# Kernel optimization log

Hardware: AMD Instinct MI355X
Metric: run time of the kernel (lower is better)

## Reference

```python
import jax, jax.numpy as jnp
import numpy as np

N_NODES = 100000
N_EDGES = 1600000
IN_DIM = 256
HID_DIM = 64
NUM_CLASSES = 32
NEG_SLOPE = 0.01  # F.leaky_relu default


def setup_inputs() -> dict:
    key = jax.random.key(0)
    k1, k2, k3, k4, k5, k6 = jax.random.split(key, 6)
    return {
        "local_features": jax.random.normal(k1, (N_NODES, IN_DIM), dtype=jnp.float32),
        "edge_index": jax.random.randint(k2, (2, N_EDGES), 0, N_NODES, dtype=jnp.int64),
        "weight1": jax.random.uniform(k3, (IN_DIM, HID_DIM), dtype=jnp.float32),
        "weight2": jax.random.uniform(k4, (HID_DIM, NUM_CLASSES), dtype=jnp.float32),
        "att_weight1": jax.random.uniform(k5, (2 * HID_DIM, 1), dtype=jnp.float32),
        "att_weight2": jax.random.uniform(k6, (2 * NUM_CLASSES, 1), dtype=jnp.float32),
    }


def _gat_attention_aggregate(H, a, src, dst, n_nodes):
    # H: [N, D], a: [2D, 1]. Edge score = leaky_relu([H_src||H_dst] @ a)
    # computed without materializing [E, 2D]: split a into src/dst halves.
    d = H.shape[1]
    s_score = (H @ a[:d]).squeeze(-1)   # [N]
    d_score = (H @ a[d:]).squeeze(-1)   # [N]
    e = jax.nn.leaky_relu(s_score[src] + d_score[dst], NEG_SLOPE)  # [E]
    # segment softmax over each row (grouped by src), as torch.sparse.softmax(dim=1)
    m = jax.ops.segment_max(e, src, num_segments=n_nodes)          # [N]
    ex = jnp.exp(e - m[src])                                       # [E]
    denom = jax.ops.segment_sum(ex, src, num_segments=n_nodes)     # [N]
    att = ex / denom[src]                                          # [E]
    # sparse mm: out[i] = sum_{(i,j) in E} att_ij * H[j]
    return jax.ops.segment_sum(att[:, None] * H[dst], src, num_segments=n_nodes)


def reference(local_features, edge_index, weight1, weight2, att_weight1, att_weight2):
    src, dst = edge_index[0], edge_index[1]
    n = local_features.shape[0]
    Hw1 = local_features @ weight1                                  # [N, HID]
    hidden = jax.nn.elu(_gat_attention_aggregate(Hw1, att_weight1, src, dst, n))
    Hw2 = hidden @ weight2                                          # [N, C]
    out = _gat_attention_aggregate(Hw2, att_weight2, src, dst, n)
    return jax.nn.log_softmax(out, axis=1)
```

## Files before the change

### kernel.cpp

```cpp
#include <hip/hip_runtime.h>
#include <math.h>

#define IN_DIM 256
#define HID 64
#define NC 32
#define NEG 0.01f
#define INF_NEG -1e30f
#define SXR 68
#define MAXNBK 512
#define SLOT 8192
#define BCAP 12288

static inline int ceil_div(int a, int b){ return (a + b - 1) / b; }

static __device__ __forceinline__ float lrelu(float x){ return x > 0.f ? x : NEG * x; }


__global__ __launch_bounds__(256) void bin_kernel(const int* __restrict__ src,
      const int* __restrict__ dst, int* __restrict__ cursor,
      unsigned int* __restrict__ tmp, int E, int nbk){
  __shared__ int hist[MAXNBK];
  __shared__ int base[MAXNBK];
  int nb = gridDim.x;
  int per = (E + nb - 1) / nb;
  int beg = blockIdx.x * per;
  int end = min(E, beg + per);
  for (int i = threadIdx.x; i < nbk; i += 256) hist[i] = 0;
  __syncthreads();
  for (int e = beg + threadIdx.x; e < end; e += 256)
    atomicAdd(&hist[src[e] >> 8], 1);
  __syncthreads();
  for (int i = threadIdx.x; i < nbk; i += 256){
    int c = hist[i];
    base[i] = (c > 0) ? atomicAdd(&cursor[i], c) : 0;
    hist[i] = 0;
  }
  __syncthreads();
  for (int e = beg + threadIdx.x; e < end; e += 256){
    int s = src[e];
    int b = s >> 8;
    int r = atomicAdd(&hist[b], 1);
    int pos = base[b] + r;
    if (pos < SLOT)
      tmp[(size_t)b * SLOT + pos] = ((unsigned)(s & 255) << 17) | (unsigned)dst[e];
  }
}

__global__ __launch_bounds__(512) void bucket_base_kernel(const int* __restrict__ cursor,
      int* __restrict__ bbase, int nbk){
  __shared__ int sh[512];
  int tid = threadIdx.x;
  int v = (tid < nbk) ? min(cursor[tid], SLOT) : 0;
  sh[tid] = v; __syncthreads();
  int val = v;
  for (int off = 1; off < 512; off <<= 1){
    int add = (tid >= off) ? sh[tid - off] : 0;
    __syncthreads();
    val += add; sh[tid] = val;
    __syncthreads();
  }
  if (tid < nbk) bbase[tid] = val - v;
}

__global__ __launch_bounds__(256) void bucket_scatter_kernel(const unsigned int* __restrict__ tmp,
      const int* __restrict__ cursor, const int* __restrict__ bbase,
      int* __restrict__ row_ptr, int* __restrict__ csr, int n){
  __shared__ int cnt[256];
  __shared__ int cur[256];
  __shared__ int lbuf[BCAP];
  int tid = threadIdx.x;
  int b = blockIdx.x;
  int n0 = b << 8;
  int nn = min(256, n - n0);
  int len = min(cursor[b], SLOT);
  int segb = bbase[b];
  const unsigned int* T = tmp + (size_t)b * SLOT;
  cnt[tid] = 0;
  __syncthreads();
  for (int e = tid; e < len; e += 256) atomicAdd(&cnt[T[e] >> 17], 1);
  __syncthreads();
  int tv = cnt[tid];
  int val = tv;
  for (int off = 1; off < 256; off <<= 1){
    int add = (tid >= off) ? cnt[tid - off] : 0;
    __syncthreads();
    val += add; cnt[tid] = val;
    __syncthreads();
  }
  int excl = val - tv;
  cur[tid] = excl;
  if (tid < nn) row_ptr[n0 + tid] = segb + excl;
  if (n0 + nn == n && tid == 0) row_ptr[n] = segb + len;
  __syncthreads();
  if (len <= BCAP){
    for (int e = tid; e < len; e += 256){
      unsigned v = T[e];
      int pos = atomicAdd(&cur[v >> 17], 1);
      lbuf[pos] = (int)(v & 0x1FFFF);
    }
    __syncthreads();
    for (int e = tid; e < len; e += 256) csr[segb + e] = lbuf[e];
  } else {
    for (int e = tid; e < len; e += 256){
      unsigned v = T[e];
      int pos = atomicAdd(&cur[v >> 17], 1);
      csr[segb + pos] = (int)(v & 0x1FFFF);
    }
  }
}


__global__ void hist_kernel(const int* __restrict__ src, int* __restrict__ counts, int E){
  int i = blockIdx.x * blockDim.x + threadIdx.x;
  if (i < E) atomicAdd(&counts[src[i]], 1);
}
__global__ void scan_blocks_kernel(const int* __restrict__ counts, int* __restrict__ excl,
                                   int* __restrict__ bsums, int n){
  __shared__ int sh[256];
  int tid = threadIdx.x;
  int base = blockIdx.x * 1024 + tid * 4;
  int c[4]; int tsum = 0;
  #pragma unroll
  for (int j = 0; j < 4; j++){ int i = base + j; c[j] = (i < n) ? counts[i] : 0; tsum += c[j]; }
  sh[tid] = tsum; __syncthreads();
  int val = tsum;
  for (int off = 1; off < 256; off <<= 1){
    int add = (tid >= off) ? sh[tid - off] : 0;
    __syncthreads();
    val += add; sh[tid] = val;
    __syncthreads();
  }
  int p = val - tsum;
  #pragma unroll
  for (int j = 0; j < 4; j++){ int i = base + j; if (i < n) excl[i] = p; p += c[j]; }
  if (tid == 255) bsums[blockIdx.x] = val;
}
__global__ void scan_sums_kernel(int* __restrict__ bsums, int* __restrict__ row_ptr,
                                 int nb, int n, int E){
  __shared__ int sh[256];
  int tid = threadIdx.x;
  int v = (tid < nb) ? bsums[tid] : 0;
  sh[tid] = v; __syncthreads();
  int val = v;
  for (int off = 1; off < 256; off <<= 1){
    int add = (tid >= off) ? sh[tid - off] : 0;
    __syncthreads();
    val += add; sh[tid] = val;
    __syncthreads();
  }
  if (tid < nb) bsums[tid] = val - v;
  if (tid == 0) row_ptr[n] = E;
}
__global__ void add_offsets_kernel(int* __restrict__ excl, const int* __restrict__ bsums, int n){
  int i = blockIdx.x * 1024 + threadIdx.x;
  if (i < n) excl[i] += bsums[blockIdx.x];
}
__global__ void scatter_kernel(const int* __restrict__ src, const int* __restrict__ dst,
                               const int* __restrict__ row_ptr, int* __restrict__ fill,
                               int* __restrict__ csr, int E){
  int i = blockIdx.x * blockDim.x + threadIdx.x;
  if (i >= E) return;
  int s = src[i];
  int pos = row_ptr[s] + atomicAdd(&fill[s], 1);
  csr[pos] = dst[i];
}


__global__ __launch_bounds__(256) void gemm1_kernel(const float* __restrict__ X, const float* __restrict__ W,
      const float* __restrict__ a, float* __restrict__ H,
      float* __restrict__ svec, float* __restrict__ dvec, int n){
  __shared__ float xs[64 * SXR];
  __shared__ float ws[64 * 64];
  int tid = threadIdx.x;
  int r0 = blockIdx.x * 64;
  int tr = tid >> 4;
  int tc = tid & 15;
  int srow = tid >> 4, sc4 = tid & 15;

  float4 pfx[4], pfw[4];
  #pragma unroll
  for (int p = 0; p < 4; p++){
    int row = p * 16 + srow;
    int gr = r0 + row;
    pfx[p] = make_float4(0.f, 0.f, 0.f, 0.f);
    if (gr < n) pfx[p] = *(const float4*)(X + (size_t)gr * IN_DIM + sc4 * 4);
    int k = p * 16 + srow;
    pfw[p] = *(const float4*)(W + (size_t)k * 64 + sc4 * 4);
  }

  float acc[4][4];
  #pragma unroll
  for (int i = 0; i < 4; i++)
    #pragma unroll
    for (int j = 0; j < 4; j++) acc[i][j] = 0.f;

  for (int kb = 0; kb < 4; kb++){
    __syncthreads();
    #pragma unroll
    for (int p = 0; p < 4; p++){
      int row = p * 16 + srow;
      *(float4*)(xs + row * SXR + sc4 * 4) = pfx[p];
      int k = p * 16 + srow;
      *(float4*)(ws + k * 64 + sc4 * 4) = pfw[p];
    }
    if (kb < 3){
      #pragma unroll
      for (int p = 0; p < 4; p++){
        int row = p * 16 + srow;
        int gr = r0 + row;
        pfx[p] = make_float4(0.f, 0.f, 0.f, 0.f);
        if (gr < n) pfx[p] = *(const float4*)(X + (size_t)gr * IN_DIM + (kb + 1) * 64 + sc4 * 4);
        int k = p * 16 + srow;
        pfw[p] = *(const float4*)(W + (size_t)((kb + 1) * 64 + k) * 64 + sc4 * 4);
      }
    }
    __syncthreads();
    #pragma unroll 2
    for (int kq = 0; kq < 16; kq++){
      float xr[4][4];
      #pragma unroll
      for (int i = 0; i < 4; i++){
        float4 v = *(const float4*)(xs + (tr * 4 + i) * SXR + kq * 4);
        xr[i][0] = v.x; xr[i][1] = v.y; xr[i][2] = v.z; xr[i][3] = v.w;
      }
      #pragma unroll
      for (int dk = 0; dk < 4; dk++){
        float4 w4 = *(const float4*)(ws + (size_t)(kq * 4 + dk) * 64 + tc * 4);
        float wv[4] = {w4.x, w4.y, w4.z, w4.w};
        #pragma unroll
        for (int i = 0; i < 4; i++)
          #pragma unroll
          for (int j = 0; j < 4; j++) acc[i][j] = fmaf(xr[i][dk], wv[j], acc[i][j]);
      }
    }
  }

  float av[4], bv[4];
  #pragma unroll
  for (int j = 0; j < 4; j++){ av[j] = a[tc * 4 + j]; bv[j] = a[64 + tc * 4 + j]; }
  float sp[4], dp[4];
  #pragma unroll
  for (int i = 0; i < 4; i++){
    float s = 0.f, d = 0.f;
    #pragma unroll
    for (int j = 0; j < 4; j++){ s = fmaf(acc[i][j], av[j], s); d = fmaf(acc[i][j], bv[j], d); }
    sp[i] = s; dp[i] = d;
  }
  #pragma unroll
  for (int off = 1; off < 16; off <<= 1){
    #pragma unroll
    for (int i = 0; i < 4; i++){
      sp[i] += __shfl_xor(sp[i], off, 16);
      dp[i] += __shfl_xor(dp[i], off, 16);
    }
  }
  #pragma unroll
  for (int i = 0; i < 4; i++){
    int r = r0 + tr * 4 + i;
    if (r < n){
      *(float4*)(H + (size_t)r * 64 + tc * 4) = make_float4(acc[i][0], acc[i][1], acc[i][2], acc[i][3]);
      if (tc == 0){ svec[r] = sp[i]; dvec[r] = dp[i]; }
    }
  }
}


__global__ __launch_bounds__(256) void gemm2_kernel(const float* __restrict__ X, const float* __restrict__ W,
      const float* __restrict__ a, float* __restrict__ H,
      float* __restrict__ svec, float* __restrict__ dvec, int n){
  __shared__ float xs[64 * SXR];
  __shared__ float ws[64 * 32];
  int tid = threadIdx.x;
  int r0 = blockIdx.x * 64;
  int tr = tid >> 4;
  int tc = tid & 15;
  int srow = tid >> 4, sc4 = tid & 15;

  #pragma unroll
  for (int p = 0; p < 4; p++){
    int row = p * 16 + srow;
    int gr = r0 + row;
    float4 v = make_float4(0.f, 0.f, 0.f, 0.f);
    if (gr < n) v = *(const float4*)(X + (size_t)gr * HID + sc4 * 4);
    *(float4*)(xs + row * SXR + sc4 * 4) = v;
  }
  #pragma unroll
  for (int p = 0; p < 2; p++){
    int idx = p * 256 + tid;
    int k = idx >> 3, c4 = idx & 7;
    *(float4*)(ws + k * 32 + c4 * 4) = *(const float4*)(W + (size_t)k * 32 + c4 * 4);
  }
  __syncthreads();

  float acc[4][2];
  #pragma unroll
  for (int i = 0; i < 4; i++){ acc[i][0] = 0.f; acc[i][1] = 0.f; }

  #pragma unroll 2
  for (int kq = 0; kq < 16; kq++){
    float xr[4][4];
    #pragma unroll
    for (int i = 0; i < 4; i++){
      float4 v = *(const float4*)(xs + (tr * 4 + i) * SXR + kq * 4);
      xr[i][0] = v.x; xr[i][1] = v.y; xr[i][2] = v.z; xr[i][3] = v.w;
    }
    #pragma unroll
    for (int dk = 0; dk < 4; dk++){
      float2 w2 = *(const float2*)(ws + (size_t)(kq * 4 + dk) * 32 + tc * 2);
      #pragma unroll
      for (int i = 0; i < 4; i++){
        acc[i][0] = fmaf(xr[i][dk], w2.x, acc[i][0]);
        acc[i][1] = fmaf(xr[i][dk], w2.y, acc[i][1]);
      }
    }
  }

  float a0 = a[tc * 2], a1 = a[tc * 2 + 1];
  float b0 = a[32 + tc * 2], b1 = a[32 + tc * 2 + 1];
  float sp[4], dp[4];
  #pragma unroll
  for (int i = 0; i < 4; i++){
    sp[i] = fmaf(acc[i][0], a0, acc[i][1] * a1);
    dp[i] = fmaf(acc[i][0], b0, acc[i][1] * b1);
  }
  #pragma unroll
  for (int off = 1; off < 16; off <<= 1){
    #pragma unroll
    for (int i = 0; i < 4; i++){
      sp[i] += __shfl_xor(sp[i], off, 16);
      dp[i] += __shfl_xor(dp[i], off, 16);
    }
  }
  #pragma unroll
  for (int i = 0; i < 4; i++){
    int r = r0 + tr * 4 + i;
    if (r < n){
      *(float2*)(H + (size_t)r * NC + tc * 2) = make_float2(acc[i][0], acc[i][1]);
      if (tc == 0){ svec[r] = sp[i]; dvec[r] = dp[i]; }
    }
  }
}


__global__ __launch_bounds__(256) void agg1_kernel(const float* __restrict__ H, const float* __restrict__ sv,
      const float* __restrict__ dv, const int* __restrict__ row_ptr, const int* __restrict__ csr,
      float* __restrict__ out, int n){
  int t = blockIdx.x * 256 + threadIdx.x;
  int g = t >> 4, fl = t & 15;
  if (g >= n) return;
  int beg = row_ptr[g], end = row_ptr[g + 1];
  float si = sv[g];
  float m = INF_NEG, l = 0.f;
  float ox = 0.f, oy = 0.f, oz = 0.f, ow = 0.f;

  for (int cb = beg; cb < end; cb += 32){
    int ce = min(cb + 32, end);
    int e0 = cb + fl, e1 = cb + 16 + fl;
    int d0 = 0, d1 = 0;
    float ev0 = INF_NEG, ev1 = INF_NEG;
    if (e0 < ce){ d0 = csr[e0]; ev0 = lrelu(si + dv[d0]); }
    if (e1 < ce){ d1 = csr[e1]; ev1 = lrelu(si + dv[d1]); }
    float lm = fmaxf(ev0, ev1);
    #pragma unroll
    for (int off = 1; off < 16; off <<= 1) lm = fmaxf(lm, __shfl_xor(lm, off, 16));
    float nm = fmaxf(m, lm);
    float alpha = __expf(m - nm);
    m = nm;
    ev0 = __expf(ev0 - nm);
    ev1 = __expf(ev1 - nm);
    float ll = ev0 + ev1;
    #pragma unroll
    for (int off = 1; off < 16; off <<= 1) ll += __shfl_xor(ll, off, 16);
    l = l * alpha + ll;
    ox *= alpha; oy *= alpha; oz *= alpha; ow *= alpha;
    #pragma unroll
    for (int jj = 0; jj < 16; jj++){
      int e = cb + jj;
      if (e >= ce) break;
      float wgt = __shfl(ev0, jj, 16);
      int dd = __shfl(d0, jj, 16);
      float4 v = *(const float4*)(H + (size_t)dd * 64 + fl * 4);
      ox = fmaf(wgt, v.x, ox); oy = fmaf(wgt, v.y, oy);
      oz = fmaf(wgt, v.z, oz); ow = fmaf(wgt, v.w, ow);
    }
    #pragma unroll
    for (int jj = 0; jj < 16; jj++){
      int e = cb + 16 + jj;
      if (e >= ce) break;
      float wgt = __shfl(ev1, jj, 16);
      int dd = __shfl(d1, jj, 16);
      float4 v = *(const float4*)(H + (size_t)dd * 64 + fl * 4);
      ox = fmaf(wgt, v.x, ox); oy = fmaf(wgt, v.y, oy);
      oz = fmaf(wgt, v.z, oz); ow = fmaf(wgt, v.w, ow);
    }
  }
  float inv = (l > 0.f) ? 1.f / l : 0.f;
  ox *= inv; oy *= inv; oz *= inv; ow *= inv;
  ox = ox > 0.f ? ox : __expf(ox) - 1.f;
  oy = oy > 0.f ? oy : __expf(oy) - 1.f;
  oz = oz > 0.f ? oz : __expf(oz) - 1.f;
  ow = ow > 0.f ? ow : __expf(ow) - 1.f;
  *(float4*)(out + (size_t)g * 64 + fl * 4) = make_float4(ox, oy, oz, ow);
}


__global__ __launch_bounds__(256) void agg2_kernel(const float* __restrict__ H, const float* __restrict__ sv,
      const float* __restrict__ dv, const int* __restrict__ row_ptr, const int* __restrict__ csr,
      float* __restrict__ out, int n){
  int t = blockIdx.x * 256 + threadIdx.x;
  int g = t >> 3, fl = t & 7;
  if (g >= n) return;
  int beg = row_ptr[g], end = row_ptr[g + 1];
  float si = sv[g];
  float m = INF_NEG, l = 0.f;
  float ox = 0.f, oy = 0.f, oz = 0.f, ow = 0.f;

  for (int cb = beg; cb < end; cb += 32){
    int ce = min(cb + 32, end);
    float ev[4]; int dd4[4];
    float lm = INF_NEG;
    #pragma unroll
    for (int s = 0; s < 4; s++){
      int e = cb + s * 8 + fl;
      ev[s] = INF_NEG; dd4[s] = 0;
      if (e < ce){ dd4[s] = csr[e]; ev[s] = lrelu(si + dv[dd4[s]]); }
      lm = fmaxf(lm, ev[s]);
    }
    #pragma unroll
    for (int off = 1; off < 8; off <<= 1) lm = fmaxf(lm, __shfl_xor(lm, off, 8));
    float nm = fmaxf(m, lm);
    float alpha = __expf(m - nm);
    m = nm;
    float ll = 0.f;
    #pragma unroll
    for (int s = 0; s < 4; s++){ ev[s] = __expf(ev[s] - nm); ll += ev[s]; }
    #pragma unroll
    for (int off = 1; off < 8; off <<= 1) ll += __shfl_xor(ll, off, 8);
    l = l * alpha + ll;
    ox *= alpha; oy *= alpha; oz *= alpha; ow *= alpha;
    #pragma unroll
    for (int s = 0; s < 4; s++){
      #pragma unroll
      for (int jj = 0; jj < 8; jj++){
        int e = cb + s * 8 + jj;
        if (e >= ce) break;
        float wgt = __shfl(ev[s], jj, 8);
        int dd = __shfl(dd4[s], jj, 8);
        float4 v = *(const float4*)(H + (size_t)dd * 32 + fl * 4);
        ox = fmaf(wgt, v.x, ox); oy = fmaf(wgt, v.y, oy);
        oz = fmaf(wgt, v.z, oz); ow = fmaf(wgt, v.w, ow);
      }
    }
  }
  float inv = (l > 0.f) ? 1.f / l : 0.f;
  ox *= inv; oy *= inv; oz *= inv; ow *= inv;
  float tm = fmaxf(fmaxf(ox, oy), fmaxf(oz, ow));
  #pragma unroll
  for (int off = 1; off < 8; off <<= 1) tm = fmaxf(tm, __shfl_xor(tm, off, 8));
  float se = __expf(ox - tm) + __expf(oy - tm) + __expf(oz - tm) + __expf(ow - tm);
  #pragma unroll
  for (int off = 1; off < 8; off <<= 1) se += __shfl_xor(se, off, 8);
  float lg = tm + __logf(se);
  *(float4*)(out + (size_t)g * 32 + fl * 4) = make_float4(ox - lg, oy - lg, oz - lg, ow - lg);
}


extern "C" void kernel_launch(void* const* d_in, const int* in_sizes, int n_in,
                              void* d_out, int out_size, void* d_ws, size_t ws_size,
                              hipStream_t stream) {
  (void)n_in; (void)out_size; (void)ws_size;
  const float* X  = (const float*)d_in[0];
  const int*   EI = (const int*)d_in[1];
  const float* W1 = (const float*)d_in[2];
  const float* W2 = (const float*)d_in[3];
  const float* A1 = (const float*)d_in[4];
  const float* A2 = (const float*)d_in[5];
  float* out = (float*)d_out;

  int N = in_sizes[0] / IN_DIM;
  int E = in_sizes[1] / 2;
  const int* src = EI;
  const int* dst = EI + E;

  auto align_up = [](size_t x){ return (x + 511) & ~(size_t)511; };
  char* w = (char*)d_ws;
  int* counts  = (int*)w;   w += align_up((size_t)N * 4);
  int* cursor  = (int*)w;   w += align_up((size_t)MAXNBK * 4);
  int* bbase   = (int*)w;   w += align_up((size_t)MAXNBK * 4);
  int* row_ptr = (int*)w;   w += align_up((size_t)(N + 1) * 4);
  int* bsums   = (int*)w;   w += align_up(1024);
  int* csr     = (int*)w;   w += align_up((size_t)E * 4);
  float* H1    = (float*)w; w += align_up((size_t)N * 64 * 4);
  float* hid   = (float*)w; w += align_up((size_t)N * 64 * 4);
  float* s1    = (float*)w; w += align_up((size_t)N * 4);
  float* d1    = (float*)w; w += align_up((size_t)N * 4);
  float* s2    = (float*)w; w += align_up((size_t)N * 4);
  float* d2    = (float*)w; w += align_up((size_t)N * 4);
  float* H2    = H1;
  unsigned int* tmp = (unsigned int*)hid;

  int nbk = ceil_div(N, 256);

  if (N <= (1 << 17) && nbk <= MAXNBK && (size_t)nbk * SLOT <= (size_t)N * 64){
    hipMemsetAsync(cursor, 0, (size_t)nbk * 4, stream);
    bin_kernel<<<256, 256, 0, stream>>>(src, dst, cursor, tmp, E, nbk);
    bucket_base_kernel<<<1, 512, 0, stream>>>(cursor, bbase, nbk);
    bucket_scatter_kernel<<<nbk, 256, 0, stream>>>(tmp, cursor, bbase, row_ptr, csr, N);
  } else {
    int nb = ceil_div(N, 1024);
    hipMemsetAsync(counts, 0, (size_t)N * 4, stream);
    hist_kernel<<<ceil_div(E, 256), 256, 0, stream>>>(src, counts, E);
    scan_blocks_kernel<<<nb, 256, 0, stream>>>(counts, row_ptr, bsums, N);
    scan_sums_kernel<<<1, 256, 0, stream>>>(bsums, row_ptr, nb, N, E);
    add_offsets_kernel<<<nb, 1024, 0, stream>>>(row_ptr, bsums, N);
    hipMemsetAsync(counts, 0, (size_t)N * 4, stream);
    scatter_kernel<<<ceil_div(E, 256), 256, 0, stream>>>(src, dst, row_ptr, counts, csr, E);
  }

  gemm1_kernel<<<ceil_div(N, 64), 256, 0, stream>>>(X, W1, A1, H1, s1, d1, N);
  agg1_kernel<<<ceil_div(N * 16, 256), 256, 0, stream>>>(H1, s1, d1, row_ptr, csr, hid, N);
  gemm2_kernel<<<ceil_div(N, 64), 256, 0, stream>>>(hid, W2, A2, H2, s2, d2, N);
  agg2_kernel<<<ceil_div(N * 8, 256), 256, 0, stream>>>(H2, s2, d2, row_ptr, csr, out, N);
}
```

Before: 396.0 us.

## Stage edge binning through LDS for coalesced writes; enlarge GEMM row tiles

```diff
diff --git a/kernel.cpp b/kernel.cpp
--- a/kernel.cpp
+++ b/kernel.cpp
@@ -8,8 +8,9 @@
 #define INF_NEG -1e30f
 #define SXR 68
 #define MAXNBK 512
-#define SLOT 8192
+#define SLOT 8256
 #define BCAP 12288
+#define BIN_CHUNK 8192
 
 static inline int ceil_div(int a, int b){ return (a + b - 1) / b; }
 
@@ -19,30 +20,57 @@
 __global__ __launch_bounds__(256) void bin_kernel(const int* __restrict__ src,
       const int* __restrict__ dst, int* __restrict__ cursor,
       unsigned int* __restrict__ tmp, int E, int nbk){
-  __shared__ int hist[MAXNBK];
-  __shared__ int base[MAXNBK];
-  int nb = gridDim.x;
-  int per = (E + nb - 1) / nb;
-  int beg = blockIdx.x * per;
-  int end = min(E, beg + per);
-  for (int i = threadIdx.x; i < nbk; i += 256) hist[i] = 0;
-  __syncthreads();
-  for (int e = beg + threadIdx.x; e < end; e += 256)
-    atomicAdd(&hist[src[e] >> 8], 1);
-  __syncthreads();
-  for (int i = threadIdx.x; i < nbk; i += 256){
-    int c = hist[i];
-    base[i] = (c > 0) ? atomicAdd(&cursor[i], c) : 0;
-    hist[i] = 0;
-  }
-  __syncthreads();
-  for (int e = beg + threadIdx.x; e < end; e += 256){
+  __shared__ unsigned int payload[BIN_CHUNK];
+  __shared__ unsigned short bid[BIN_CHUNK];
+  __shared__ int cnt[MAXNBK];
+  __shared__ int lofs[MAXNBK];
+  __shared__ int gbase[MAXNBK];
+  __shared__ int s2[256];
+  int tid = threadIdx.x;
+  int beg = blockIdx.x * BIN_CHUNK;
+  int end = min(E, beg + BIN_CHUNK);
+  int len = end - beg;
+
+  for (int i = tid; i < MAXNBK; i += 256) cnt[i] = 0;
+  __syncthreads();
+  for (int e = beg + tid; e < end; e += 256)
+    atomicAdd(&cnt[src[e] >> 8], 1);
+  __syncthreads();
+  int a0 = cnt[2 * tid], a1 = cnt[2 * tid + 1];
+  int pair = a0 + a1;
+  s2[tid] = pair; __syncthreads();
+  int val = pair;
+  for (int off = 1; off < 256; off <<= 1){
+    int add = (tid >= off) ? s2[tid - off] : 0;
+    __syncthreads();
+    val += add; s2[tid] = val;
+    __syncthreads();
+  }
+  int ep = val - pair;
+  lofs[2 * tid] = ep;
+  lofs[2 * tid + 1] = ep + a0;
+  __syncthreads();
+  for (int i = tid; i < nbk; i += 256){
+    int c = cnt[i];
+    gbase[i] = (c > 0) ? atomicAdd(&cursor[i], c) : 0;
+  }
+  __syncthreads();
+  for (int i = tid; i < MAXNBK; i += 256) cnt[i] = 0;
+  __syncthreads();
+  for (int e = beg + tid; e < end; e += 256){
     int s = src[e];
     int b = s >> 8;
-    int r = atomicAdd(&hist[b], 1);
-    int pos = base[b] + r;
-    if (pos < SLOT)
-      tmp[(size_t)b * SLOT + pos] = ((unsigned)(s & 255) << 17) | (unsigned)dst[e];
+    int r = atomicAdd(&cnt[b], 1);
+    int pos = lofs[b] + r;
+    payload[pos] = ((unsigned)(s & 255) << 17) | (unsigned)dst[e];
+    bid[pos] = (unsigned short)b;
+  }
+  __syncthreads();
+  for (int pos = tid; pos < len; pos += 256){
+    int b = bid[pos];
+    int idx = pos - lofs[b];
+    int g = gbase[b] + idx;
+    if (g < SLOT) tmp[(size_t)b * SLOT + g] = payload[pos];
   }
 }
 
@@ -169,58 +197,66 @@
 __global__ __launch_bounds__(256) void gemm1_kernel(const float* __restrict__ X, const float* __restrict__ W,
       const float* __restrict__ a, float* __restrict__ H,
       float* __restrict__ svec, float* __restrict__ dvec, int n){
-  __shared__ float xs[64 * SXR];
+  __shared__ float xs[128 * SXR];
   __shared__ float ws[64 * 64];
   int tid = threadIdx.x;
-  int r0 = blockIdx.x * 64;
+  int r0 = blockIdx.x * 128;
   int tr = tid >> 4;
   int tc = tid & 15;
   int srow = tid >> 4, sc4 = tid & 15;
 
-  float4 pfx[4], pfw[4];
-  #pragma unroll
-  for (int p = 0; p < 4; p++){
+  float4 pfx[8], pfw[4];
+  #pragma unroll
+  for (int p = 0; p < 8; p++){
     int row = p * 16 + srow;
     int gr = r0 + row;
     pfx[p] = make_float4(0.f, 0.f, 0.f, 0.f);
     if (gr < n) pfx[p] = *(const float4*)(X + (size_t)gr * IN_DIM + sc4 * 4);
+  }
+  #pragma unroll
+  for (int p = 0; p < 4; p++){
     int k = p * 16 + srow;
     pfw[p] = *(const float4*)(W + (size_t)k * 64 + sc4 * 4);
   }
 
-  float acc[4][4];
-  #pragma unroll
-  for (int i = 0; i < 4; i++)
+  float acc[8][4];
+  #pragma unroll
+  for (int i = 0; i < 8; i++)
     #pragma unroll
     for (int j = 0; j < 4; j++) acc[i][j] = 0.f;
 
   for (int kb = 0; kb < 4; kb++){
     __syncthreads();
     #pragma unroll
-    for (int p = 0; p < 4; p++){
+    for (int p = 0; p < 8; p++){
       int row = p * 16 + srow;
       *(float4*)(xs + row * SXR + sc4 * 4) = pfx[p];
+    }
+    #pragma unroll
+    for (int p = 0; p < 4; p++){
       int k = p * 16 + srow;
       *(float4*)(ws + k * 64 + sc4 * 4) = pfw[p];
     }
     if (kb < 3){
       #pragma unroll
-      for (int p = 0; p < 4; p++){
+      for (int p = 0; p < 8; p++){
         int row = p * 16 + srow;
         int gr = r0 + row;
         pfx[p] = make_float4(0.f, 0.f, 0.f, 0.f);
         if (gr < n) pfx[p] = *(const float4*)(X + (size_t)gr * IN_DIM + (kb + 1) * 64 + sc4 * 4);
+      }
+      #pragma unroll
+      for (int p = 0; p < 4; p++){
         int k = p * 16 + srow;
         pfw[p] = *(const float4*)(W + (size_t)((kb + 1) * 64 + k) * 64 + sc4 * 4);
       }
     }
     __syncthreads();
-    #pragma unroll 2
     for (int kq = 0; kq < 16; kq++){
-      float xr[4][4];
+      float xr[8][4];
       #pragma unroll
-      for (int i = 0; i < 4; i++){
-        float4 v = *(const float4*)(xs + (tr * 4 + i) * SXR + kq * 4);
+      for (int i = 0; i < 8; i++){
+        float4 v = *(const float4*)(xs + (tr * 8 + i) * SXR + kq * 4);
         xr[i][0] = v.x; xr[i][1] = v.y; xr[i][2] = v.z; xr[i][3] = v.w;
       }
       #pragma unroll
@@ -228,7 +264,7 @@
         float4 w4 = *(const float4*)(ws + (size_t)(kq * 4 + dk) * 64 + tc * 4);
         float wv[4] = {w4.x, w4.y, w4.z, w4.w};
         #pragma unroll
-        for (int i = 0; i < 4; i++)
+        for (int i = 0; i < 8; i++)
           #pragma unroll
           for (int j = 0; j < 4; j++) acc[i][j] = fmaf(xr[i][dk], wv[j], acc[i][j]);
       }
@@ -238,9 +274,9 @@
   float av[4], bv[4];
   #pragma unroll
   for (int j = 0; j < 4; j++){ av[j] = a[tc * 4 + j]; bv[j] = a[64 + tc * 4 + j]; }
-  float sp[4], dp[4];
-  #pragma unroll
-  for (int i = 0; i < 4; i++){
+  float sp[8], dp[8];
+  #pragma unroll
+  for (int i = 0; i < 8; i++){
     float s = 0.f, d = 0.f;
     #pragma unroll
     for (int j = 0; j < 4; j++){ s = fmaf(acc[i][j], av[j], s); d = fmaf(acc[i][j], bv[j], d); }
@@ -249,14 +285,14 @@
   #pragma unroll
   for (int off = 1; off < 16; off <<= 1){
     #pragma unroll
-    for (int i = 0; i < 4; i++){
+    for (int i = 0; i < 8; i++){
       sp[i] += __shfl_xor(sp[i], off, 16);
       dp[i] += __shfl_xor(dp[i], off, 16);
     }
   }
   #pragma unroll
-  for (int i = 0; i < 4; i++){
-    int r = r0 + tr * 4 + i;
+  for (int i = 0; i < 8; i++){
+    int r = r0 + tr * 8 + i;
     if (r < n){
       *(float4*)(H + (size_t)r * 64 + tc * 4) = make_float4(acc[i][0], acc[i][1], acc[i][2], acc[i][3]);
       if (tc == 0){ svec[r] = sp[i]; dvec[r] = dp[i]; }
@@ -268,16 +304,16 @@
 __global__ __launch_bounds__(256) void gemm2_kernel(const float* __restrict__ X, const float* __restrict__ W,
       const float* __restrict__ a, float* __restrict__ H,
       float* __restrict__ svec, float* __restrict__ dvec, int n){
-  __shared__ float xs[64 * SXR];
+  __shared__ float xs[128 * SXR];
   __shared__ float ws[64 * 32];
   int tid = threadIdx.x;
-  int r0 = blockIdx.x * 64;
+  int r0 = blockIdx.x * 128;
   int tr = tid >> 4;
   int tc = tid & 15;
   int srow = tid >> 4, sc4 = tid & 15;
 
   #pragma unroll
-  for (int p = 0; p < 4; p++){
+  for (int p = 0; p < 8; p++){
     int row = p * 16 + srow;
     int gr = r0 + row;
     float4 v = make_float4(0.f, 0.f, 0.f, 0.f);
@@ -292,23 +328,22 @@
   }
   __syncthreads();
 
-  float acc[4][2];
-  #pragma unroll
-  for (int i = 0; i < 4; i++){ acc[i][0] = 0.f; acc[i][1] = 0.f; }
-
-  #pragma unroll 2
+  float acc[8][2];
+  #pragma unroll
+  for (int i = 0; i < 8; i++){ acc[i][0] = 0.f; acc[i][1] = 0.f; }
+
   for (int kq = 0; kq < 16; kq++){
-    float xr[4][4];
-    #pragma unroll
-    for (int i = 0; i < 4; i++){
-      float4 v = *(const float4*)(xs + (tr * 4 + i) * SXR + kq * 4);
+    float xr[8][4];
+    #pragma unroll
+    for (int i = 0; i < 8; i++){
+      float4 v = *(const float4*)(xs + (tr * 8 + i) * SXR + kq * 4);
       xr[i][0] = v.x; xr[i][1] = v.y; xr[i][2] = v.z; xr[i][3] = v.w;
     }
     #pragma unroll
     for (int dk = 0; dk < 4; dk++){
       float2 w2 = *(const float2*)(ws + (size_t)(kq * 4 + dk) * 32 + tc * 2);
       #pragma unroll
-      for (int i = 0; i < 4; i++){
+      for (int i = 0; i < 8; i++){
         acc[i][0] = fmaf(xr[i][dk], w2.x, acc[i][0]);
         acc[i][1] = fmaf(xr[i][dk], w2.y, acc[i][1]);
       }
@@ -317,23 +352,23 @@
 
   float a0 = a[tc * 2], a1 = a[tc * 2 + 1];
   float b0 = a[32 + tc * 2], b1 = a[32 + tc * 2 + 1];
-  float sp[4], dp[4];
-  #pragma unroll
-  for (int i = 0; i < 4; i++){
+  float sp[8], dp[8];
+  #pragma unroll
+  for (int i = 0; i < 8; i++){
     sp[i] = fmaf(acc[i][0], a0, acc[i][1] * a1);
     dp[i] = fmaf(acc[i][0], b0, acc[i][1] * b1);
   }
   #pragma unroll
   for (int off = 1; off < 16; off <<= 1){
     #pragma unroll
-    for (int i = 0; i < 4; i++){
+    for (int i = 0; i < 8; i++){
       sp[i] += __shfl_xor(sp[i], off, 16);
       dp[i] += __shfl_xor(dp[i], off, 16);
     }
   }
   #pragma unroll
-  for (int i = 0; i < 4; i++){
-    int r = r0 + tr * 4 + i;
+  for (int i = 0; i < 8; i++){
+    int r = r0 + tr * 8 + i;
     if (r < n){
       *(float2*)(H + (size_t)r * NC + tc * 2) = make_float2(acc[i][0], acc[i][1]);
       if (tc == 0){ svec[r] = sp[i]; dvec[r] = dp[i]; }
@@ -503,7 +538,7 @@
 
   if (N <= (1 << 17) && nbk <= MAXNBK && (size_t)nbk * SLOT <= (size_t)N * 64){
     hipMemsetAsync(cursor, 0, (size_t)nbk * 4, stream);
-    bin_kernel<<<256, 256, 0, stream>>>(src, dst, cursor, tmp, E, nbk);
+    bin_kernel<<<ceil_div(E, BIN_CHUNK), 256, 0, stream>>>(src, dst, cursor, tmp, E, nbk);
     bucket_base_kernel<<<1, 512, 0, stream>>>(cursor, bbase, nbk);
     bucket_scatter_kernel<<<nbk, 256, 0, stream>>>(tmp, cursor, bbase, row_ptr, csr, N);
   } else {
@@ -517,8 +552,8 @@
     scatter_kernel<<<ceil_div(E, 256), 256, 0, stream>>>(src, dst, row_ptr, counts, csr, E);
   }
 
-  gemm1_kernel<<<ceil_div(N, 64), 256, 0, stream>>>(X, W1, A1, H1, s1, d1, N);
+  gemm1_kernel<<<ceil_div(N, 128), 256, 0, stream>>>(X, W1, A1, H1, s1, d1, N);
   agg1_kernel<<<ceil_div(N * 16, 256), 256, 0, stream>>>(H1, s1, d1, row_ptr, csr, hid, N);
-  gemm2_kernel<<<ceil_div(N, 64), 256, 0, stream>>>(hid, W2, A2, H2, s2, d2, N);
+  gemm2_kernel<<<ceil_div(N, 128), 256, 0, stream>>>(hid, W2, A2, H2, s2, d2, N);
   agg2_kernel<<<ceil_div(N * 8, 256), 256, 0, stream>>>(H2, s2, d2, row_ptr, csr, out, N);
 }
```

Result: no change. 390.8 us (-1.3%).
